# Kernel optimization log

Measured on AMD Instinct MI355X. Metric: run time of the kernel, lower is better.

## Reference

```python
import jax, jax.numpy as jnp
import numpy as np

B, N, M = 8, 131072, 64
M_VALID = 48  # trailing padding, matches remove_pad semantics
POSITIVE_IOU = 0.5
NEGATIVE_IOU = 0.3
CLASS_NUM = 1  # hardcoded in RpnTarget.__init__


def _make_boxes(key, shape_prefix, max_wh=64.0, span=1024.0):
    k1, k2, k3, k4 = jax.random.split(key, 4)
    x1 = jax.random.uniform(k1, shape_prefix, minval=0.0, maxval=span)
    y1 = jax.random.uniform(k2, shape_prefix, minval=0.0, maxval=span)
    w = jax.random.uniform(k3, shape_prefix, minval=4.0, maxval=max_wh)
    h = jax.random.uniform(k4, shape_prefix, minval=4.0, maxval=max_wh)
    return jnp.stack([x1, y1, x1 + w, y1 + h], axis=-1)


def setup_inputs() -> dict:
    key = jax.random.key(0)
    ka, kb = jax.random.split(key, 2)
    prior_anchors = _make_boxes(ka, (B, N))                       # [B,N,4]
    boxes = _make_boxes(kb, (B, M), max_wh=128.0)                 # [B,M,4]
    status = jnp.concatenate(
        [jnp.ones((B, M_VALID, 1)), jnp.zeros((B, M - M_VALID, 1))], axis=1
    )
    gt_bboxes = jnp.concatenate([boxes, status], axis=-1)          # [B,M,5]
    gt_class_idxes = jnp.zeros((B, M, 2), dtype=jnp.int32)         # zeroed in call()
    return {
        "prior_anchors": prior_anchors,
        "gt_bboxes": gt_bboxes,
        "gt_class_idxes": gt_class_idxes,
    }


def _bbox_transform(anchors, bboxes):
    # anchors, bboxes: [..., 4] in [x1,y1,x2,y2]
    ax = (anchors[..., 0] + anchors[..., 2]) * 0.5
    ay = (anchors[..., 1] + anchors[..., 3]) * 0.5
    aw = anchors[..., 2] - anchors[..., 0]
    ah = anchors[..., 3] - anchors[..., 1]
    bx = (bboxes[..., 0] + bboxes[..., 2]) * 0.5
    by = (bboxes[..., 1] + bboxes[..., 3]) * 0.5
    bw = bboxes[..., 2] - bboxes[..., 0]
    bh = bboxes[..., 3] - bboxes[..., 1]
    tx = (bx - ax) / aw
    ty = (by - ay) / ah
    tw = jnp.log(bw / aw)
    th = jnp.log(bh / ah)
    return jnp.stack([tx, ty, tw, th], axis=-1)


def _rpn_targets(prior_anchors, gt_bboxes, gt_class_idxes):
    boxes = gt_bboxes[..., :4]                 # [B,M,4]
    valid = gt_bboxes[..., 4] > 0              # [B,M] padding status

    a = prior_anchors[:, :, None, :]           # [B,N,1,4]
    b = boxes[:, None, :, :]                   # [B,1,M,4]
    inter_w = jnp.maximum(jnp.minimum(a[..., 2], b[..., 2]) - jnp.maximum(a[..., 0], b[..., 0]), 0.0)
    inter_h = jnp.maximum(jnp.minimum(a[..., 3], b[..., 3]) - jnp.maximum(a[..., 1], b[..., 1]), 0.0)
    inter = inter_w * inter_h                  # [B,N,M]
    area_a = jnp.maximum(a[..., 2] - a[..., 0], 0.0) * jnp.maximum(a[..., 3] - a[..., 1], 0.0)
    area_b = jnp.maximum(b[..., 2] - b[..., 0], 0.0) * jnp.maximum(b[..., 3] - b[..., 1], 0.0)
    iou = inter / (area_a + area_b - inter)    # [B,N,M]
    # mask out padded gt boxes (equivalent to remove_pad + trailing padding)
    iou = jnp.where(valid[:, None, :], iou, -1.0)

    max_iou = jnp.max(iou, axis=-1)            # [B,N]
    match_idx = jnp.argmax(iou, axis=-1)       # [B,N]
    positive = max_iou >= POSITIVE_IOU
    ignore = (max_iou >= NEGATIVE_IOU) & ~positive

    matched_boxes = jnp.take_along_axis(boxes, match_idx[..., None], axis=1)  # [B,N,4]
    reg = _bbox_transform(prior_anchors, matched_boxes)                        # [B,N,4]

    status = jnp.where(positive, 1.0, jnp.where(ignore, -1.0, 0.0))[..., None]  # [B,N,1]

    # call() zeros gt_class_idxes, so matched class idx is always 0; one_hot depth 1 -> ones
    cls_idx = jnp.take_along_axis(
        jnp.zeros_like(gt_class_idxes)[..., 0], match_idx, axis=1
    )                                                                           # [B,N] int32 zeros
    cls = jax.nn.one_hot(cls_idx, CLASS_NUM, dtype=reg.dtype)                   # [B,N,1]

    regression_targets = jnp.concatenate([reg, status], axis=-1)                # [B,N,5]
    classification_targets = jnp.concatenate([cls, status], axis=-1)            # [B,N,2]
    return regression_targets, classification_targets


def reference(prior_anchors, gt_bboxes, gt_class_idxes):
    return _rpn_targets(prior_anchors, gt_bboxes, gt_class_idxes)
```

## Files before the change

kernel.cpp:

```cpp
#include <hip/hip_runtime.h>


#define BB    8
#define NN    131072
#define MM    64
#define BLK   256
#define NBLK  (NN / BLK)
#define GC    16
#define CELLS (GC * GC)

#define WS_BOXES 0
#define WS_CNT   8192
#define WS_L8    8224
#define WS_LEN   24608

typedef unsigned long long u64;
typedef unsigned char u8;

__global__ __launch_bounds__(256) void rpn_build_lists(
    const float* __restrict__ gt, char* __restrict__ ws)
{
    __shared__ float4 sbox[MM];
    __shared__ int    scnt;

    const int b = blockIdx.x;
    const int t = threadIdx.x;

    float4* wboxes = (float4*)(ws + WS_BOXES);
    int*    wcnt   = (int*)(ws + WS_CNT);
    u64*    wl8    = (u64*)(ws + WS_L8);
    u8*     wlen   = (u8*)(ws + WS_LEN);

    if (t < MM) {
        const float* g = gt + ((size_t)b * MM + t) * 5;
        float x1 = g[0], y1 = g[1], x2 = g[2], y2 = g[3], st = g[4];
        bool valid = (st > 0.0f);
        u64 mask = __ballot(valid);
        int slot = __popcll(mask & ((1ull << t) - 1ull));
        int cntL = __popcll(mask);
        if (t == 0) { scnt = cntL; wcnt[b] = cntL; }
        if (valid) {
            float4 bx = make_float4(x1, y1, x2, y2);
            sbox[slot] = bx;
            wboxes[b * MM + slot] = bx;
        }
        if (t >= cntL)
            wboxes[b * MM + t] = make_float4(0.f, 0.f, 0.f, 0.f);
    }
    __syncthreads();

    const int cnt = scnt;
    const int cx = t & (GC - 1), cy = t >> 4;
    const float wx1 = cx * 64.0f, wx2 = wx1 + 128.0f;
    const float wy1 = cy * 64.0f, wy2 = wy1 + 128.0f;

    u64 l8 = ~0ull;
    int len = 0;
    for (int s = 0; s < cnt; ++s) {
        float4 bx = sbox[s];
        if (bx.x <= wx2 && bx.z >= wx1 && bx.y <= wy2 && bx.w >= wy1) {
            if (len < 8) {
                const int sh = 8 * len;
                l8 = (l8 & ~(0xFFull << sh)) | ((u64)s << sh);
            }
            ++len;
        }
    }
    wl8[(size_t)b * CELLS + t]  = l8;
    wlen[(size_t)b * CELLS + t] = (u8)len;
}

__global__ __launch_bounds__(BLK) void rpn_target_kernel(
    const float* __restrict__ anchors,
    const float* __restrict__ gt,
    const char* __restrict__ ws,
    float* __restrict__ out)
{
    constexpr float INV = GC / 1024.0f;

    __shared__ float sreg[BLK * 5];

    const int t = threadIdx.x;
    const int b = blockIdx.x / NBLK;
    const int n = (blockIdx.x % NBLK) * BLK + t;

    const float4* wboxes = (const float4*)(ws + WS_BOXES) + (size_t)b * MM;

    const float4 a = ((const float4*)anchors)[(size_t)b * NN + n];

    int cx = (int)(a.x * INV); cx = cx < 0 ? 0 : (cx > GC - 1 ? GC - 1 : cx);
    int cy = (int)(a.y * INV); cy = cy < 0 ? 0 : (cy > GC - 1 ? GC - 1 : cy);
    const int cid = cy * GC + cx;

    const u64 lst8 = ((const u64*)(ws + WS_L8))[(size_t)b * CELLS + cid];
    const int cnt  = ((const int*)(ws + WS_CNT))[b];

    const float area_a = fmaxf(a.z - a.x, 0.0f) * fmaxf(a.w - a.y, 0.0f);

    float  best = 0.0f;
    float4 mb   = wboxes[0];

    float  iou[8];
    float4 cb[8];
    #pragma unroll
    for (int j = 0; j < 8; ++j) {
        const int raw = (int)((lst8 >> (8 * j)) & 0xFFull);
        const int idx = raw & 63;
        const float4 bb = wboxes[idx];
        cb[j] = bb;
        float iw = fmaxf(fminf(a.z, bb.z) - fmaxf(a.x, bb.x), 0.0f);
        float ih = fmaxf(fminf(a.w, bb.w) - fmaxf(a.y, bb.y), 0.0f);
        float inter = iw * ih;
        inter = (raw != 255) ? inter : 0.0f;
        float ab = fmaxf(bb.z - bb.x, 0.0f) * fmaxf(bb.w - bb.y, 0.0f);
        float denom = (area_a + ab) - inter;
        iou[j] = inter / denom;
    }
    #pragma unroll
    for (int j = 0; j < 8; ++j)
        if (iou[j] > best) { best = iou[j]; mb = cb[j]; }

    if (__any(((lst8 >> 56) & 0xFFull) != 0xFFull)) {
        const int len = ((const u8*)(ws + WS_LEN))[(size_t)b * CELLS + cid];
        if (len > 8) {
            best = 0.0f; mb = wboxes[0];
            for (int j = 0; j < cnt; ++j) {
                const float4 bb = wboxes[j];
                float iw = fmaxf(fminf(a.z, bb.z) - fmaxf(a.x, bb.x), 0.0f);
                float ih = fmaxf(fminf(a.w, bb.w) - fmaxf(a.y, bb.y), 0.0f);
                float inter = iw * ih;
                float ab = fmaxf(bb.z - bb.x, 0.0f) * fmaxf(bb.w - bb.y, 0.0f);
                float denom = (area_a + ab) - inter;
                float iou = inter / denom;
                if (iou > best) { best = iou; mb = bb; }
            }
        }
    }

    const float status = (best >= 0.5f) ? 1.0f : ((best >= 0.3f) ? -1.0f : 0.0f);

    if (cnt == 0) {
        const float* g0 = gt + (size_t)b * MM * 5;
        mb = make_float4(g0[0], g0[1], g0[2], g0[3]);
    }

    const float aw  = a.z - a.x;
    const float ah  = a.w - a.y;
    const float rw  = __builtin_amdgcn_rcpf(aw);
    const float rh  = __builtin_amdgcn_rcpf(ah);
    const float tx  = ((mb.x + mb.z) * 0.5f - (a.x + a.z) * 0.5f) * rw;
    const float ty  = ((mb.y + mb.w) * 0.5f - (a.y + a.w) * 0.5f) * rh;
    const float LN2 = 0.69314718055994531f;
    const float tw  = __builtin_amdgcn_logf((mb.z - mb.x) * rw) * LN2;
    const float th  = __builtin_amdgcn_logf((mb.w - mb.y) * rh) * LN2;

    sreg[t * 5 + 0] = tx;
    sreg[t * 5 + 1] = ty;
    sreg[t * 5 + 2] = tw;
    sreg[t * 5 + 3] = th;
    sreg[t * 5 + 4] = status;
    __syncthreads();

    const size_t regbase = ((size_t)b * NN + (size_t)(blockIdx.x % NBLK) * BLK) * 5;
    #pragma unroll
    for (int k = 0; k < 5; ++k)
        out[regbase + (size_t)k * BLK + t] = sreg[k * BLK + t];

    const size_t gid = (size_t)b * NN + n;
    float2* c = (float2*)(out + (size_t)BB * NN * 5) + gid;
    *c = make_float2(1.0f, status);
}

extern "C" void kernel_launch(void* const* d_in, const int* in_sizes, int n_in,
                              void* d_out, int out_size, void* d_ws, size_t ws_size,
                              hipStream_t stream) {
    const float* anchors = (const float*)d_in[0];
    const float* gt      = (const float*)d_in[1];

    float* out = (float*)d_out;
    char*  ws  = (char*)d_ws;

    hipLaunchKernelGGL(rpn_build_lists, dim3(BB), dim3(256), 0, stream, gt, ws);
    hipLaunchKernelGGL(rpn_target_kernel, dim3(BB * NBLK), dim3(BLK), 0, stream,
                       anchors, gt, ws, out);
}
```

Measured before the change: 27.34 us.

## Store candidate boxes per grid cell and refine grid to 32x32

The per-cell candidate lists now hold the eight box coordinates directly instead of byte indices. This removes the dependent gather through the index list in the target kernel. The grid becomes a template parameter: a 32x32 grid is used when the workspace is large enough, otherwise 8x8, with the list-building work spread across more blocks. The LDS transpose for the regression output is replaced by direct strided 5-float stores, which drops a barrier but gives less coalesced writes. Each cell now costs 128 bytes of workspace, read once per anchor.

```diff
diff --git a/kernel.cpp b/kernel.cpp
--- a/kernel.cpp
+++ b/kernel.cpp
@@ -6,30 +6,31 @@
 #define MM    64
 #define BLK   256
 #define NBLK  (NN / BLK)
-#define GC    16
-#define CELLS (GC * GC)
-
-#define WS_BOXES 0
-#define WS_CNT   8192
-#define WS_L8    8224
-#define WS_LEN   24608
 
 typedef unsigned long long u64;
 typedef unsigned char u8;
 
-__global__ __launch_bounds__(256) void rpn_build_lists(
+#define WS_BOXES 0
+#define WS_CNT   8192
+#define WS_CB    8256
+
+template<int GC>
+__global__ __launch_bounds__(256) void rpn_build_cells(
     const float* __restrict__ gt, char* __restrict__ ws)
 {
+    constexpr int CELLS = GC * GC;
+    constexpr int CPB   = (CELLS + 255) / 256;
+    constexpr float SCALE = 1024.0f / GC;
+
     __shared__ float4 sbox[MM];
     __shared__ int    scnt;
 
-    const int b = blockIdx.x;
-    const int t = threadIdx.x;
+    const int b  = blockIdx.x / CPB;
+    const int cg = blockIdx.x % CPB;
+    const int t  = threadIdx.x;
 
     float4* wboxes = (float4*)(ws + WS_BOXES);
     int*    wcnt   = (int*)(ws + WS_CNT);
-    u64*    wl8    = (u64*)(ws + WS_L8);
-    u8*     wlen   = (u8*)(ws + WS_LEN);
 
     if (t < MM) {
         const float* g = gt + ((size_t)b * MM + t) * 5;
@@ -38,53 +39,63 @@
         u64 mask = __ballot(valid);
         int slot = __popcll(mask & ((1ull << t) - 1ull));
         int cntL = __popcll(mask);
-        if (t == 0) { scnt = cntL; wcnt[b] = cntL; }
-        if (valid) {
-            float4 bx = make_float4(x1, y1, x2, y2);
-            sbox[slot] = bx;
-            wboxes[b * MM + slot] = bx;
+        if (t == 0) { scnt = cntL; if (cg == 0) wcnt[b] = cntL; }
+        if (cg == 0) {
+            if (valid) wboxes[b * MM + slot] = make_float4(x1, y1, x2, y2);
+            if (t >= cntL) wboxes[b * MM + t] = make_float4(0.f, 0.f, 0.f, 0.f);
         }
-        if (t >= cntL)
-            wboxes[b * MM + t] = make_float4(0.f, 0.f, 0.f, 0.f);
+        if (valid) sbox[slot] = make_float4(x1, y1, x2, y2);
     }
     __syncthreads();
 
-    const int cnt = scnt;
-    const int cx = t & (GC - 1), cy = t >> 4;
-    const float wx1 = cx * 64.0f, wx2 = wx1 + 128.0f;
-    const float wy1 = cy * 64.0f, wy2 = wy1 + 128.0f;
+    const int cnt  = scnt;
+    const int cell = cg * 256 + t;
+    if (cell >= CELLS) return;
 
-    u64 l8 = ~0ull;
+    const int cx = cell & (GC - 1), cy = cell / GC;
+    const float wx1 = cx * SCALE, wx2 = wx1 + (SCALE + 64.0f);
+    const float wy1 = cy * SCALE, wy2 = wy1 + (SCALE + 64.0f);
+
+    float4 c0 = make_float4(0,0,0,0), c1 = c0, c2 = c0, c3 = c0;
+    float4 c4 = c0, c5 = c0, c6 = c0, c7 = c0;
     int len = 0;
     for (int s = 0; s < cnt; ++s) {
         float4 bx = sbox[s];
         if (bx.x <= wx2 && bx.z >= wx1 && bx.y <= wy2 && bx.w >= wy1) {
-            if (len < 8) {
-                const int sh = 8 * len;
-                l8 = (l8 & ~(0xFFull << sh)) | ((u64)s << sh);
+            switch (len) {
+                case 0: c0 = bx; break;
+                case 1: c1 = bx; break;
+                case 2: c2 = bx; break;
+                case 3: c3 = bx; break;
+                case 4: c4 = bx; break;
+                case 5: c5 = bx; break;
+                case 6: c6 = bx; break;
+                case 7: c7 = bx; break;
+                default: break;
             }
             ++len;
         }
     }
-    wl8[(size_t)b * CELLS + t]  = l8;
-    wlen[(size_t)b * CELLS + t] = (u8)len;
+    if (len > 8) c7 = make_float4(-1.f, -1.f, -1.f, -1.f);
+
+    float4* cbp = (float4*)(ws + WS_CB) + ((size_t)b * CELLS + cell) * 8;
+    cbp[0] = c0; cbp[1] = c1; cbp[2] = c2; cbp[3] = c3;
+    cbp[4] = c4; cbp[5] = c5; cbp[6] = c6; cbp[7] = c7;
 }
 
+template<int GC>
 __global__ __launch_bounds__(BLK) void rpn_target_kernel(
     const float* __restrict__ anchors,
     const float* __restrict__ gt,
     const char* __restrict__ ws,
     float* __restrict__ out)
 {
+    constexpr int CELLS = GC * GC;
     constexpr float INV = GC / 1024.0f;
-
-    __shared__ float sreg[BLK * 5];
 
     const int t = threadIdx.x;
     const int b = blockIdx.x / NBLK;
     const int n = (blockIdx.x % NBLK) * BLK + t;
-
-    const float4* wboxes = (const float4*)(ws + WS_BOXES) + (size_t)b * MM;
 
     const float4 a = ((const float4*)anchors)[(size_t)b * NN + n];
 
@@ -92,37 +103,39 @@
     int cy = (int)(a.y * INV); cy = cy < 0 ? 0 : (cy > GC - 1 ? GC - 1 : cy);
     const int cid = cy * GC + cx;
 
-    const u64 lst8 = ((const u64*)(ws + WS_L8))[(size_t)b * CELLS + cid];
-    const int cnt  = ((const int*)(ws + WS_CNT))[b];
+    const float4* cbp = (const float4*)(ws + WS_CB) + ((size_t)b * CELLS + cid) * 8;
+    float4 c[8];
+    #pragma unroll
+    for (int j = 0; j < 8; ++j) c[j] = cbp[j];
 
     const float area_a = fmaxf(a.z - a.x, 0.0f) * fmaxf(a.w - a.y, 0.0f);
+    const int cnt = ((const int*)(ws + WS_CNT))[b];
 
-    float  best = 0.0f;
-    float4 mb   = wboxes[0];
-
-    float  iou[8];
-    float4 cb[8];
+    float iou[8];
     #pragma unroll
     for (int j = 0; j < 8; ++j) {
-        const int raw = (int)((lst8 >> (8 * j)) & 0xFFull);
-        const int idx = raw & 63;
-        const float4 bb = wboxes[idx];
-        cb[j] = bb;
+        const float4 bb = c[j];
         float iw = fmaxf(fminf(a.z, bb.z) - fmaxf(a.x, bb.x), 0.0f);
         float ih = fmaxf(fminf(a.w, bb.w) - fmaxf(a.y, bb.y), 0.0f);
         float inter = iw * ih;
-        inter = (raw != 255) ? inter : 0.0f;
         float ab = fmaxf(bb.z - bb.x, 0.0f) * fmaxf(bb.w - bb.y, 0.0f);
         float denom = (area_a + ab) - inter;
         iou[j] = inter / denom;
     }
+    float  best = 0.0f;
+    float4 mb;
+    {
+        const float4* wboxes = (const float4*)(ws + WS_BOXES) + (size_t)b * MM;
+        mb = wboxes[0];
+    }
     #pragma unroll
     for (int j = 0; j < 8; ++j)
-        if (iou[j] > best) { best = iou[j]; mb = cb[j]; }
+        if (iou[j] > best) { best = iou[j]; mb = c[j]; }
 
-    if (__any(((lst8 >> 56) & 0xFFull) != 0xFFull)) {
-        const int len = ((const u8*)(ws + WS_LEN))[(size_t)b * CELLS + cid];
-        if (len > 8) {
+    const bool ovf = (c[7].x < 0.0f);
+    if (__any(ovf)) {
+        if (ovf) {
+            const float4* wboxes = (const float4*)(ws + WS_BOXES) + (size_t)b * MM;
             best = 0.0f; mb = wboxes[0];
             for (int j = 0; j < cnt; ++j) {
                 const float4 bb = wboxes[j];
@@ -131,8 +144,8 @@
                 float inter = iw * ih;
                 float ab = fmaxf(bb.z - bb.x, 0.0f) * fmaxf(bb.w - bb.y, 0.0f);
                 float denom = (area_a + ab) - inter;
-                float iou = inter / denom;
-                if (iou > best) { best = iou; mb = bb; }
+                float iou2 = inter / denom;
+                if (iou2 > best) { best = iou2; mb = bb; }
             }
         }
     }
@@ -154,21 +167,13 @@
     const float tw  = __builtin_amdgcn_logf((mb.z - mb.x) * rw) * LN2;
     const float th  = __builtin_amdgcn_logf((mb.w - mb.y) * rh) * LN2;
 
-    sreg[t * 5 + 0] = tx;
-    sreg[t * 5 + 1] = ty;
-    sreg[t * 5 + 2] = tw;
-    sreg[t * 5 + 3] = th;
-    sreg[t * 5 + 4] = status;
-    __syncthreads();
+    const size_t gid = (size_t)b * NN + n;
 
-    const size_t regbase = ((size_t)b * NN + (size_t)(blockIdx.x % NBLK) * BLK) * 5;
-    #pragma unroll
-    for (int k = 0; k < 5; ++k)
-        out[regbase + (size_t)k * BLK + t] = sreg[k * BLK + t];
+    float* r = out + gid * 5;
+    r[0] = tx; r[1] = ty; r[2] = tw; r[3] = th; r[4] = status;
 
-    const size_t gid = (size_t)b * NN + n;
-    float2* c = (float2*)(out + (size_t)BB * NN * 5) + gid;
-    *c = make_float2(1.0f, status);
+    float2* cc = (float2*)(out + (size_t)BB * NN * 5) + gid;
+    *cc = make_float2(1.0f, status);
 }
 
 extern "C" void kernel_launch(void* const* d_in, const int* in_sizes, int n_in,
@@ -180,7 +185,14 @@
     float* out = (float*)d_out;
     char*  ws  = (char*)d_ws;
 
-    hipLaunchKernelGGL(rpn_build_lists, dim3(BB), dim3(256), 0, stream, gt, ws);
-    hipLaunchKernelGGL(rpn_target_kernel, dim3(BB * NBLK), dim3(BLK), 0, stream,
-                       anchors, gt, ws, out);
+    const size_t need32 = 8256 + (size_t)BB * 32 * 32 * 128;
+    if (ws_size >= need32) {
+        hipLaunchKernelGGL((rpn_build_cells<32>), dim3(BB * 4), dim3(256), 0, stream, gt, ws);
+        hipLaunchKernelGGL((rpn_target_kernel<32>), dim3(BB * NBLK), dim3(BLK), 0, stream,
+                           anchors, gt, ws, out);
+    } else {
+        hipLaunchKernelGGL((rpn_build_cells<8>), dim3(BB), dim3(256), 0, stream, gt, ws);
+        hipLaunchKernelGGL((rpn_target_kernel<8>), dim3(BB * NBLK), dim3(BLK), 0, stream,
+                           anchors, gt, ws, out);
+    }
 }
```

New measurement: 42.19 us. 1.54x slower.
